# Kernel optimization log

Hardware: AMD Instinct MI355X
Metric: run time of the kernel (lower is better)

Reference implementation:

```python
import jax, jax.numpy as jnp
import numpy as np
import math

B, N, T, H, HEADS, FIN, NL_TR = 4, 256, 16, 128, 4, 2, 5
M = B * N
NEG = -1e9

def _sinusoidal(t, h):
    pos = jnp.arange(t, dtype=jnp.float32)[:, None]
    div = jnp.exp(jnp.arange(0, h, 2, dtype=jnp.float32) * (-math.log(10000.0) / h))
    pe = jnp.zeros((t, h), dtype=jnp.float32)
    pe = pe.at[:, 0::2].set(jnp.sin(pos * div))
    pe = pe.at[:, 1::2].set(jnp.cos(pos * div))
    return pe

def _gat(x, W, a_src, a_dst, b, E, m):
    # x: [T,M,F]; W: [F,heads,H]; E: [T,M,M] bool, E[t,i,j]=edge j->i; m: [T,M] bool
    h = jnp.einsum('tmf,fhd->tmhd', x, W)
    ss = jnp.einsum('tmhd,hd->tmh', h, a_src)  # source score per node
    sd = jnp.einsum('tmhd,hd->tmh', h, a_dst)  # dest score per node
    logits = jax.nn.leaky_relu(sd[:, :, None, :] + ss[:, None, :, :], 0.2)  # [T,i,j,h]
    logits = jnp.where(E[..., None], logits, NEG)
    alpha = jax.nn.softmax(logits, axis=2)  # segment-softmax over incoming edges
    out = jnp.einsum('tijh,tjhd->tihd', alpha, h).mean(axis=2) + b  # concat=False -> head mean + bias
    return jax.nn.relu(out) * m[..., None]

def _ln(x, s, b):
    mu = x.mean(-1, keepdims=True)
    v = ((x - mu) ** 2).mean(-1, keepdims=True)
    return (x - mu) / jnp.sqrt(v + 1e-5) * s + b

def _forward(ego_mask, positions, adjacency, gat1_W, gat1_asrc, gat1_adst, gat1_b, gatW, gat_asrc, gat_adst, gat_b, Wqkv, bqkv, Wo, bo, ln1_s, ln1_b, ln2_s, ln2_b, Wff1, bff1, Wff2, bff2):
    m = jnp.transpose(ego_mask, (1, 0, 2)).reshape(T, M)  # [T, B*N]
    eye = jnp.eye(M, dtype=bool)
    # edge j->i valid iff A[t,j,i]!=0 and both nodes masked; PyG GATConv adds self-loops
    E = ((jnp.swapaxes(adjacency, 1, 2) != 0) & m[:, :, None] & m[:, None, :]) | (eye[None] & m[:, :, None])
    x = _gat(positions, gat1_W, gat1_asrc, gat1_adst, gat1_b, E, m)
    for i in range(5):
        x = _gat(x, gatW[i], gat_asrc[i], gat_adst[i], gat_b[i], E, m)
    x_seq = jnp.transpose(x, (1, 0, 2)) + _sinusoidal(T, H)[None]  # [M, T, H]
    dh = H // HEADS
    scale = 1.0 / math.sqrt(dh)
    for l in range(NL_TR):
        q = (x_seq @ Wqkv[l, 0] + bqkv[l, 0]).reshape(M, T, HEADS, dh)
        k = (x_seq @ Wqkv[l, 1] + bqkv[l, 1]).reshape(M, T, HEADS, dh)
        v = (x_seq @ Wqkv[l, 2] + bqkv[l, 2]).reshape(M, T, HEADS, dh)
        sc = jnp.einsum('bqhd,bkhd->bhqk', q, k) * scale
        a = jax.nn.softmax(sc, axis=-1)
        o = jnp.einsum('bhqk,bkhd->bqhd', a, v).reshape(M, T, H) @ Wo[l] + bo[l]
        x_seq = _ln(x_seq + o, ln1_s[l], ln1_b[l])
        f = jax.nn.relu(x_seq @ Wff1[l] + bff1[l]) @ Wff2[l] + bff2[l]
        x_seq = _ln(x_seq + f, ln2_s[l], ln2_b[l])
    return x_seq.reshape(B, N, T, H)

def setup_inputs() -> dict:
    key = jax.random.key(0)
    ks = jax.random.split(key, 32)
    s = 0.05
    f32 = jnp.float32
    inp = {
        'ego_mask': jax.random.uniform(ks[0], (B, T, N)) < 0.95,
        'positions': jax.random.normal(ks[1], (T, M, FIN), dtype=f32),
        'adjacency': (jax.random.uniform(ks[2], (T, M, M)) < 0.02).astype(f32),
        'gat1_W': jax.random.normal(ks[3], (FIN, HEADS, H), dtype=f32) * s,
        'gat1_asrc': jax.random.normal(ks[4], (HEADS, H), dtype=f32) * s,
        'gat1_adst': jax.random.normal(ks[5], (HEADS, H), dtype=f32) * s,
        'gat1_b': jnp.zeros((H,), dtype=f32),
        'gatW': jax.random.normal(ks[6], (5, H, HEADS, H), dtype=f32) * s,
        'gat_asrc': jax.random.normal(ks[7], (5, HEADS, H), dtype=f32) * s,
        'gat_adst': jax.random.normal(ks[8], (5, HEADS, H), dtype=f32) * s,
        'gat_b': jnp.zeros((5, H), dtype=f32),
        'Wqkv': jax.random.normal(ks[9], (NL_TR, 3, H, H), dtype=f32) * s,
        'bqkv': jnp.zeros((NL_TR, 3, H), dtype=f32),
        'Wo': jax.random.normal(ks[10], (NL_TR, H, H), dtype=f32) * s,
        'bo': jnp.zeros((NL_TR, H), dtype=f32),
        'ln1_s': jnp.ones((NL_TR, H), dtype=f32),
        'ln1_b': jnp.zeros((NL_TR, H), dtype=f32),
        'ln2_s': jnp.ones((NL_TR, H), dtype=f32),
        'ln2_b': jnp.zeros((NL_TR, H), dtype=f32),
        'Wff1': jax.random.normal(ks[11], (NL_TR, H, 4 * H), dtype=f32) * s,
        'bff1': jnp.zeros((NL_TR, 4 * H), dtype=f32),
        'Wff2': jax.random.normal(ks[12], (NL_TR, 4 * H, H), dtype=f32) * s,
        'bff2': jnp.zeros((NL_TR, H), dtype=f32),
    }
    return inp

def reference(ego_mask, positions, adjacency, gat1_W, gat1_asrc, gat1_adst, gat1_b, gatW, gat_asrc, gat_adst, gat_b, Wqkv, bqkv, Wo, bo, ln1_s, ln1_b, ln2_s, ln2_b, Wff1, bff1, Wff2, bff2):
    return _forward(ego_mask, positions, adjacency, gat1_W, gat1_asrc, gat1_adst, gat1_b, gatW, gat_asrc, gat_adst, gat_b, Wqkv, bqkv, Wo, bo, ln1_s, ln1_b, ln2_s, ln2_b, Wff1, bff1, Wff2, bff2)
```

## Files before the change

### kernel.cpp

```cpp
#include <hip/hip_runtime.h>
#include <hip/hip_bf16.h>

#define TT 16
#define MM 1024
#define HDIM 128
#define NHEADS 4
#define NROWS (TT*MM)
#define MAXDEG 64

typedef __bf16 bf16x8 __attribute__((ext_vector_type(8)));
typedef float f32x4 __attribute__((ext_vector_type(4)));

__device__ __forceinline__ unsigned short f2b(float x) {
    unsigned u = __float_as_uint(x);
    u += 0x7fff + ((u >> 16) & 1);
    return (unsigned short)(u >> 16);
}
__device__ __forceinline__ float bu2f(unsigned short u) {
    return __uint_as_float(((unsigned)u) << 16);
}

__global__ __launch_bounds__(256) void k_init(const int* __restrict__ ego,
                                              float* __restrict__ mfl,
                                              int* __restrict__ cnt) {
    int idx = blockIdx.x * 256 + threadIdx.x;
    int t = idx >> 10, i = idx & 1023;
    int b = i >> 8, n = i & 255;
    mfl[idx] = ego[b * (TT * 256) + t * 256 + n] ? 1.f : 0.f;
    cnt[idx] = 0;
}

__global__ __launch_bounds__(256) void k_edges(const float* __restrict__ adj,
                                               const float* __restrict__ mfl,
                                               int* __restrict__ cnt,
                                               int* __restrict__ nbr) {
    int bid = blockIdx.x;
    int t = bid >> 6, jc = bid & 63;
    int tid = threadIdx.x;
    int i0 = tid * 4;
    int rowb = t * MM;
    float mi[4];
#pragma unroll
    for (int r = 0; r < 4; ++r) mi[r] = mfl[rowb + i0 + r];
    __shared__ float ms[16];
    if (tid < 16) ms[tid] = mfl[rowb + jc * 16 + tid];
    __syncthreads();
    const float* at = adj + (size_t)t * MM * MM;
#pragma unroll 4
    for (int jj = 0; jj < 16; ++jj) {
        int j = jc * 16 + jj;
        float4 a = *(const float4*)(at + (size_t)j * MM + i0);
        float mj = ms[jj];
#pragma unroll
        for (int r = 0; r < 4; ++r) {
            int i = i0 + r;
            bool e;
            if (j == i) e = (mi[r] != 0.f);
            else e = ((&a.x)[r] != 0.f) && (mj != 0.f) && (mi[r] != 0.f);
            if (e) {
                int row = rowb + i;
                int pos = atomicAdd(&cnt[row], 1);
                if (pos < MAXDEG) nbr[(size_t)row * MAXDEG + pos] = j;
            }
        }
    }
}

__global__ __launch_bounds__(256) void k_prep(const float* __restrict__ Wqkv,
                                              const float* __restrict__ Wo,
                                              const float* __restrict__ Wff1,
                                              const float* __restrict__ Wff2,
                                              const float* __restrict__ gW,
                                              unsigned short* __restrict__ Wb) {
    int o = blockIdx.x * 256 + threadIdx.x;
    const float* src; int cs;
    if (o < 122880) {
        int l = o / 24576, r = o % 24576;
        if (r < 6144) {
            int nt = r >> 8, rem = r & 255, ks = rem >> 6, lane = rem & 63;
            int mt = nt >> 3, cc = nt & 7;
            int k = ks * 32 + ((lane >> 4) << 3), c = cc * 16 + (lane & 15);
            src = Wqkv + ((size_t)(l * 3 + mt) * 128 + k) * 128 + c; cs = 128;
        } else if (r < 8192) {
            int u = r - 6144, nt = u >> 8, rem = u & 255, ks = rem >> 6, lane = rem & 63;
            int k = ks * 32 + ((lane >> 4) << 3), c = nt * 16 + (lane & 15);
            src = Wo + (size_t)l * 16384 + (size_t)k * 128 + c; cs = 128;
        } else if (r < 16384) {
            int u = r - 8192, nt = u >> 8, rem = u & 255, ks = rem >> 6, lane = rem & 63;
            int k = ks * 32 + ((lane >> 4) << 3), c = nt * 16 + (lane & 15);
            src = Wff1 + (size_t)l * 65536 + (size_t)k * 512 + c; cs = 512;
        } else {
            int u = r - 16384, nt = u >> 10, rem = u & 1023, ks = rem >> 6, lane = rem & 63;
            int k = ks * 32 + ((lane >> 4) << 3), c = nt * 16 + (lane & 15);
            src = Wff2 + (size_t)l * 65536 + (size_t)k * 128 + c; cs = 128;
        }
    } else {
        int u = o - 122880;
        int l = u >> 13, rr = u & 8191;
        int nt = rr >> 8, rem = rr & 255, ks = rem >> 6, lane = rem & 63;
        int k = ks * 32 + ((lane >> 4) << 3), c = nt * 16 + (lane & 15);
        src = gW + (size_t)l * 65536 + (size_t)k * 512 + c; cs = 512;
    }
    unsigned v[4];
#pragma unroll
    for (int j = 0; j < 4; ++j)
        v[j] = (unsigned)f2b(src[(2 * j) * (size_t)cs]) |
               ((unsigned)f2b(src[(2 * j + 1) * (size_t)cs]) << 16);
    *(uint4*)(Wb + (size_t)o * 8) = make_uint4(v[0], v[1], v[2], v[3]);
}

__global__ __launch_bounds__(128) void k_gat1(const float* __restrict__ x,
                                              const float* __restrict__ W,
                                              const float* __restrict__ asrc,
                                              const float* __restrict__ adst,
                                              unsigned short* __restrict__ h16,
                                              float* __restrict__ ss,
                                              float* __restrict__ sd) {
    int bid = blockIdx.x;
    int row = ((bid & 7) << 11) + (bid >> 3);
    int tid = threadIdx.x;
    float x0 = x[row * 2], x1 = x[row * 2 + 1];
    float s4[4], d4[4];
#pragma unroll
    for (int hh = 0; hh < 4; ++hh) {
        int o = hh * 128 + tid;
        float v = x0 * W[o] + x1 * W[512 + o];
        h16[(size_t)row * 512 + o] = f2b(v);
        s4[hh] = v * asrc[o];
        d4[hh] = v * adst[o];
    }
#pragma unroll
    for (int hh = 0; hh < 4; ++hh)
        for (int off = 32; off; off >>= 1) {
            s4[hh] += __shfl_down(s4[hh], off, 64);
            d4[hh] += __shfl_down(d4[hh], off, 64);
        }
    __shared__ float red[2][2][4];
    if ((tid & 63) == 0) {
        int w = tid >> 6;
#pragma unroll
        for (int hh = 0; hh < 4; ++hh) { red[w][0][hh] = s4[hh]; red[w][1][hh] = d4[hh]; }
    }
    __syncthreads();
    if (tid < 4) ss[row * 4 + tid] = red[0][0][tid] + red[1][0][tid];
    else if (tid < 8) sd[row * 4 + tid - 4] = red[0][1][tid - 4] + red[1][1][tid - 4];
}

__global__ __launch_bounds__(256, 2) void k_gat_h(const unsigned short* __restrict__ x16,
                                                  const unsigned short* __restrict__ Wg,
                                                  const float* __restrict__ asrc,
                                                  const float* __restrict__ adst,
                                                  unsigned short* __restrict__ h16,
                                                  float* __restrict__ ss,
                                                  float* __restrict__ sd) {
    __shared__ __align__(16) unsigned short xb[32 * 136];
    int bid = blockIdx.x;
    int row0 = (((bid & 7) << 6) + (bid >> 3)) * 32;
    int tid = threadIdx.x;
#pragma unroll
    for (int q = 0; q < 2; ++q) {
        int u = tid + q * 256;
        int rr = u >> 4, cc = (u & 15) * 8;
        *(uint4*)(xb + rr * 136 + cc) = *(const uint4*)(x16 + (size_t)(row0 + rr) * 128 + cc);
    }
    __syncthreads();
    const int lane = tid & 63, w = tid >> 6;
    const int mrow = lane & 15, quad = lane >> 4;
    float ps[2][4] = {{0,0,0,0},{0,0,0,0}}, pd[2][4] = {{0,0,0,0},{0,0,0,0}};
#pragma unroll
    for (int ib = 0; ib < 4; ++ib) {
        bf16x8 wb[8];
#pragma unroll
        for (int u = 0; u < 2; ++u) {
            int nt = w * 8 + ib * 2 + u;
#pragma unroll
            for (int ks = 0; ks < 4; ++ks)
                wb[u * 4 + ks] = *(const bf16x8*)(Wg + (size_t)((nt * 4 + ks) * 64 + lane) * 8);
        }
#pragma unroll
        for (int rg = 0; rg < 2; ++rg) {
            bf16x8 af[4];
#pragma unroll
            for (int ks = 0; ks < 4; ++ks)
                af[ks] = *(const bf16x8*)(xb + (rg * 16 + mrow) * 136 + ks * 32 + quad * 8);
            f32x4 acc[2];
            acc[0] = (f32x4){0.f, 0.f, 0.f, 0.f};
            acc[1] = (f32x4){0.f, 0.f, 0.f, 0.f};
#pragma unroll
            for (int u = 0; u < 2; ++u)
#pragma unroll
                for (int ks = 0; ks < 4; ++ks)
                    acc[u] = __builtin_amdgcn_mfma_f32_16x16x32_bf16(af[ks], wb[u * 4 + ks], acc[u], 0, 0, 0);
#pragma unroll
            for (int u = 0; u < 2; ++u) {
                int nt = w * 8 + ib * 2 + u, col = nt * 16 + mrow;
                float as_ = asrc[col], ad_ = adst[col];
#pragma unroll
                for (int r = 0; r < 4; ++r) {
                    float v = acc[u][r];
                    h16[(size_t)(row0 + rg * 16 + quad * 4 + r) * 512 + col] = f2b(v);
                    ps[rg][r] += v * as_; pd[rg][r] += v * ad_;
                }
            }
        }
    }
#pragma unroll
    for (int off = 1; off < 16; off <<= 1)
#pragma unroll
        for (int rg = 0; rg < 2; ++rg)
#pragma unroll
            for (int r = 0; r < 4; ++r) {
                ps[rg][r] += __shfl_xor(ps[rg][r], off, 64);
                pd[rg][r] += __shfl_xor(pd[rg][r], off, 64);
            }
    if (mrow == 0) {
#pragma unroll
        for (int rg = 0; rg < 2; ++rg)
#pragma unroll
            for (int r = 0; r < 4; ++r) {
                int row = row0 + rg * 16 + quad * 4 + r;
                ss[row * 4 + w] = ps[rg][r];
                sd[row * 4 + w] = pd[rg][r];
            }
    }
}

__global__ __launch_bounds__(256, 2) void k_agg(const unsigned short* __restrict__ h16,
                                                const float* __restrict__ ss,
                                                const float* __restrict__ sd,
                                                const int* __restrict__ cnt,
                                                const int* __restrict__ nbr,
                                                const float* __restrict__ mfl,
                                                const float* __restrict__ bias,
                                                unsigned short* __restrict__ xo16) {
    __shared__ float alB[4][MAXDEG][4];
    __shared__ int   nbB[4][MAXDEG];
    __shared__ __align__(16) float partB[4][512];
    int bid = blockIdx.x;
    int row0 = (((bid & 7) << 9) + (bid >> 3)) * 4;
    int tid = threadIdx.x;
    const int w = tid >> 6, lane = tid & 63;
    int row = row0 + w, t = row >> 10;
    bool valid = mfl[row] != 0.f;
    int c = 0;
    if (valid) { c = cnt[row]; if (c > MAXDEG) c = MAXDEG; }
    bool act = lane < c;
    int jreg = 0;
    float lg[4];
    if (act) {
        jreg = nbr[(size_t)row * MAXDEG + lane];
        int jr = t * MM + jreg;
#pragma unroll
        for (int hh = 0; hh < 4; ++hh) {
            float v = sd[row * 4 + hh] + ss[jr * 4 + hh];
            lg[hh] = v > 0.f ? v : 0.2f * v;
        }
    } else {
#pragma unroll
        for (int hh = 0; hh < 4; ++hh) lg[hh] = -1e30f;
    }
    float mx[4];
#pragma unroll
    for (int hh = 0; hh < 4; ++hh) mx[hh] = lg[hh];
#pragma unroll
    for (int off = 32; off; off >>= 1)
#pragma unroll
        for (int hh = 0; hh < 4; ++hh) mx[hh] = fmaxf(mx[hh], __shfl_xor(mx[hh], off, 64));
    float ev[4];
#pragma unroll
    for (int hh = 0; hh < 4; ++hh) ev[hh] = act ? __expf(lg[hh] - mx[hh]) : 0.f;
    float sm[4];
#pragma unroll
    for (int hh = 0; hh < 4; ++hh) sm[hh] = ev[hh];
#pragma unroll
    for (int off = 32; off; off >>= 1)
#pragma unroll
        for (int hh = 0; hh < 4; ++hh) sm[hh] += __shfl_xor(sm[hh], off, 64);
    if (act) {
        float4 a4 = make_float4(ev[0] / sm[0], ev[1] / sm[1], ev[2] / sm[2], ev[3] / sm[3]);
        *(float4*)&alB[w][lane][0] = a4;
        nbB[w][lane] = jreg;
    }
    __syncthreads();
    const int head = lane >> 4;
    float acc[8] = {0, 0, 0, 0, 0, 0, 0, 0};
    const unsigned short* hb = h16 + (size_t)t * MM * 512 + lane * 8;
    for (int n = 0; n < c; ++n) {
        int j = nbB[w][n];
        float a = alB[w][n][head];
        uint4 v = *(const uint4*)(hb + (size_t)j * 512);
        acc[0] += a * bu2f((unsigned short)(v.x & 0xffff));
        acc[1] += a * bu2f((unsigned short)(v.x >> 16));
        acc[2] += a * bu2f((unsigned short)(v.y & 0xffff));
        acc[3] += a * bu2f((unsigned short)(v.y >> 16));
        acc[4] += a * bu2f((unsigned short)(v.z & 0xffff));
        acc[5] += a * bu2f((unsigned short)(v.z >> 16));
        acc[6] += a * bu2f((unsigned short)(v.w & 0xffff));
        acc[7] += a * bu2f((unsigned short)(v.w >> 16));
    }
    *(float4*)&partB[w][lane * 8]     = make_float4(acc[0], acc[1], acc[2], acc[3]);
    *(float4*)&partB[w][lane * 8 + 4] = make_float4(acc[4], acc[5], acc[6], acc[7]);
    __syncthreads();
    {
        int d0 = lane * 2;
        unsigned outp = 0;
#pragma unroll
        for (int q = 0; q < 2; ++q) {
            int d = d0 + q;
            float v = 0.f;
            if (valid) {
                v = 0.25f * (partB[w][d] + partB[w][128 + d] + partB[w][256 + d] + partB[w][384 + d])
                    + bias[d];
                v = fmaxf(v, 0.f);
            }
            outp |= ((unsigned)f2b(v)) << (16 * q);
        }
        *(unsigned*)(xo16 + (size_t)row * 128 + d0) = outp;
    }
}

__device__ __forceinline__ void ln2x(float* xs, unsigned short* xbB,
                                     const float* s, const float* b) {
    int tid = threadIdx.x, lane = tid & 15;
#pragma unroll
    for (int half = 0; half < 2; ++half) {
        int rr = (tid >> 4) + half * 16;
        float* xr = xs + rr * 128;
        float sum = 0.f;
#pragma unroll
        for (int k2 = 0; k2 < 8; ++k2) sum += xr[lane + 16 * k2];
#pragma unroll
        for (int off = 8; off; off >>= 1) sum += __shfl_xor(sum, off, 16);
        float mean = sum * (1.f / 128.f);
        float vs = 0.f;
#pragma unroll
        for (int k2 = 0; k2 < 8; ++k2) { float d = xr[lane + 16 * k2] - mean; vs += d * d; }
#pragma unroll
        for (int off = 8; off; off >>= 1) vs += __shfl_xor(vs, off, 16);
        float rstd = rsqrtf(vs * (1.f / 128.f) + 1e-5f);
        unsigned short* xb = xbB + (rr >> 4) * 2176 + (rr & 15) * 136;
#pragma unroll
        for (int k2 = 0; k2 < 8; ++k2) {
            int d = lane + 16 * k2;
            float v = (xr[d] - mean) * rstd * s[d] + b[d];
            xr[d] = v;
            xb[d] = f2b(v);
        }
    }
    __syncthreads();
}

__global__ __launch_bounds__(256, 2) void k_tf(const unsigned short* __restrict__ xg,
        const unsigned short* __restrict__ Wb,
        const float* __restrict__ bqkv, const float* __restrict__ bo,
        const float* __restrict__ ln1s, const float* __restrict__ ln1b,
        const float* __restrict__ ln2s, const float* __restrict__ ln2b,
        const float* __restrict__ bff1, const float* __restrict__ bff2,
        float* __restrict__ out) {
    __shared__ __align__(16) float smem[16640];
    float* xs  = smem;
    float* sbB = smem + 4096;
    unsigned short* xbB  = (unsigned short*)(smem + 6144);
    unsigned short* qkvB = (unsigned short*)(smem + 8320);
    const int m0 = blockIdx.x * 2, tid = threadIdx.x;
    const int lane = tid & 63, w = tid >> 6;
    const int mrow = lane & 15, quad = lane >> 4;

    for (int idx = tid; idx < 4096; idx += 256) {
        int sq = idx >> 11, t = (idx >> 7) & 15, d = idx & 127, jj = d >> 1;
        float arg = (float)t * expf(-(float)(2 * jj) * (9.210340371976184f / 128.f));
        float pe = (d & 1) ? cosf(arg) : sinf(arg);
        xs[idx] = bu2f(xg[(size_t)t * (MM * HDIM) + (size_t)(m0 + sq) * HDIM + d]) + pe;
    }
    __syncthreads();
#pragma unroll
    for (int half = 0; half < 2; ++half) {
        int u = tid + half * 256;
        int rr = u >> 4, cc = (u & 15) * 8;
        const float* xp = xs + rr * 128 + cc;
        unsigned v[4];
#pragma unroll
        for (int j = 0; j < 4; ++j)
            v[j] = (unsigned)f2b(xp[2 * j]) | ((unsigned)f2b(xp[2 * j + 1]) << 16);
        *(uint4*)(xbB + (rr >> 4) * 2176 + (rr & 15) * 136 + cc) = make_uint4(v[0], v[1], v[2], v[3]);
    }
    __syncthreads();

    for (int l = 0; l < 5; ++l) {
        const unsigned short* Wl = Wb + (size_t)l * 196608;
        {
            bf16x8 af[2][4];
#pragma unroll
            for (int sid = 0; sid < 2; ++sid)
#pragma unroll
                for (int ks = 0; ks < 4; ++ks)
                    af[sid][ks] = *(const bf16x8*)(xbB + sid * 2176 + mrow * 136 + ks * 32 + quad * 8);
#pragma unroll
            for (int ib = 0; ib < 3; ++ib) {
                bf16x8 wb[8];
#pragma unroll
                for (int u = 0; u < 2; ++u) {
                    int nt = w * 6 + ib * 2 + u;
                    const unsigned short* bp = Wl + (size_t)(nt * 4) * 512 + lane * 8;
#pragma unroll
                    for (int ks = 0; ks < 4; ++ks)
                        wb[u * 4 + ks] = *(const bf16x8*)(bp + ks * 512);
                }
                f32x4 acc[2][2];
#pragma unroll
                for (int sid = 0; sid < 2; ++sid)
#pragma unroll
                    for (int u = 0; u < 2; ++u) acc[sid][u] = (f32x4){0.f, 0.f, 0.f, 0.f};
#pragma unroll
                for (int sid = 0; sid < 2; ++sid)
#pragma unroll
                    for (int u = 0; u < 2; ++u)
#pragma unroll
                        for (int ks = 0; ks < 4; ++ks)
                            acc[sid][u] = __builtin_amdgcn_mfma_f32_16x16x32_bf16(af[sid][ks], wb[u * 4 + ks], acc[sid][u], 0, 0, 0);
#pragma unroll
                for (int sid = 0; sid < 2; ++sid)
#pragma unroll
                    for (int u = 0; u < 2; ++u) {
                        int nt = w * 6 + ib * 2 + u, mt = nt >> 3, cc = nt & 7;
                        int col = cc * 16 + mrow;
                        float bb = bqkv[l * 384 + mt * 128 + col];
                        unsigned short* dst = qkvB + sid * 6528 + mt * 2176;
#pragma unroll
                        for (int r = 0; r < 4; ++r)
                            dst[(quad * 4 + r) * 136 + col] = f2b(acc[sid][u][r] + bb);
                    }
            }
        }
        __syncthreads();
        {
            int hh = tid >> 6, tq = (tid >> 2) & 15, tk0 = (tid & 3) * 4;
#pragma unroll
            for (int sid = 0; sid < 2; ++sid) {
                const unsigned short* qp = qkvB + sid * 6528 + tq * 136 + hh * 32;
                const unsigned short* kb = qkvB + sid * 6528 + 2176;
                float a[4] = {0.f, 0.f, 0.f, 0.f};
#pragma unroll
                for (int d4 = 0; d4 < 4; ++d4) {
                    uint4 qv = *(const uint4*)(qp + d4 * 8);
                    float qf[8];
                    qf[0] = bu2f((unsigned short)(qv.x & 0xffff)); qf[1] = bu2f((unsigned short)(qv.x >> 16));
                    qf[2] = bu2f((unsigned short)(qv.y & 0xffff)); qf[3] = bu2f((unsigned short)(qv.y >> 16));
                    qf[4] = bu2f((unsigned short)(qv.z & 0xffff)); qf[5] = bu2f((unsigned short)(qv.z >> 16));
                    qf[6] = bu2f((unsigned short)(qv.w & 0xffff)); qf[7] = bu2f((unsigned short)(qv.w >> 16));
#pragma unroll
                    for (int j = 0; j < 4; ++j) {
                        uint4 kv = *(const uint4*)(kb + (tk0 + j) * 136 + hh * 32 + d4 * 8);
                        a[j] += qf[0] * bu2f((unsigned short)(kv.x & 0xffff));
                        a[j] += qf[1] * bu2f((unsigned short)(kv.x >> 16));
                        a[j] += qf[2] * bu2f((unsigned short)(kv.y & 0xffff));
                        a[j] += qf[3] * bu2f((unsigned short)(kv.y >> 16));
                        a[j] += qf[4] * bu2f((unsigned short)(kv.z & 0xffff));
                        a[j] += qf[5] * bu2f((unsigned short)(kv.z >> 16));
                        a[j] += qf[6] * bu2f((unsigned short)(kv.w & 0xffff));
                        a[j] += qf[7] * bu2f((unsigned short)(kv.w >> 16));
                    }
                }
#pragma unroll
                for (int j = 0; j < 4; ++j)
                    sbB[sid * 1024 + (tk0 + j) * 64 + hh * 16 + tq] = a[j] * 0.17677669529663687f;
            }
        }
        __syncthreads();
        if (tid < 128) {
            float* sbp = sbB + (tid >> 6) * 1024;
            int cc = tid & 63;
            float mx = -1e30f;
#pragma unroll
            for (int u = 0; u < 16; ++u) mx = fmaxf(mx, sbp[u * 64 + cc]);
            float s = 0.f;
#pragma unroll
            for (int u = 0; u < 16; ++u) { float e = __expf(sbp[u * 64 + cc] - mx); sbp[u * 64 + cc] = e; s += e; }
            float inv = 1.f / s;
#pragma unroll
            for (int u = 0; u < 16; ++u) sbp[u * 64 + cc] *= inv;
        }
        __syncthreads();
        {
            int o = tid & 127, r0p = (tid >> 7) * 8, hh = o >> 5;
#pragma unroll
            for (int sid = 0; sid < 2; ++sid) {
                const unsigned short* vb = qkvB + sid * 6528 + 4352;
                const float* sb = sbB + sid * 1024;
                float accp[8] = {0, 0, 0, 0, 0, 0, 0, 0};
                for (int u = 0; u < 16; ++u) {
                    float vv = bu2f(vb[u * 136 + o]);
                    const float* pp = sb + u * 64 + hh * 16 + r0p;
#pragma unroll
                    for (int r = 0; r < 8; ++r) accp[r] += pp[r] * vv;
                }
#pragma unroll
                for (int r = 0; r < 8; ++r)
                    xbB[sid * 2176 + (r0p + r) * 136 + o] = f2b(accp[r]);
            }
        }
        __syncthreads();
        {
            bf16x8 af[2][4];
#pragma unroll
            for (int sid = 0; sid < 2; ++sid)
#pragma unroll
                for (int ks = 0; ks < 4; ++ks)
                    af[sid][ks] = *(const bf16x8*)(xbB + sid * 2176 + mrow * 136 + ks * 32 + quad * 8);
            const unsigned short* Ws = Wl + 49152;
            bf16x8 wb[8];
#pragma unroll
            for (int u = 0; u < 2; ++u) {
                int nt = w * 2 + u;
#pragma unroll
                for (int ks = 0; ks < 4; ++ks)
                    wb[u * 4 + ks] = *(const bf16x8*)(Ws + (size_t)((nt * 4 + ks) * 64 + lane) * 8);
            }
            f32x4 acc[2][2];
#pragma unroll
            for (int sid = 0; sid < 2; ++sid)
#pragma unroll
                for (int u = 0; u < 2; ++u) acc[sid][u] = (f32x4){0.f, 0.f, 0.f, 0.f};
#pragma unroll
            for (int sid = 0; sid < 2; ++sid)
#pragma unroll
                for (int u = 0; u < 2; ++u)
#pragma unroll
                    for (int ks = 0; ks < 4; ++ks)
                        acc[sid][u] = __builtin_amdgcn_mfma_f32_16x16x32_bf16(af[sid][ks], wb[u * 4 + ks], acc[sid][u], 0, 0, 0);
#pragma unroll
            for (int sid = 0; sid < 2; ++sid)
#pragma unroll
                for (int u = 0; u < 2; ++u) {
                    int col = (w * 2 + u) * 16 + mrow;
                    float bb = bo[l * 128 + col];
#pragma unroll
                    for (int r = 0; r < 4; ++r)
                        xs[sid * 2048 + (quad * 4 + r) * 128 + col] += acc[sid][u][r] + bb;
                }
        }
        __syncthreads();
        ln2x(xs, xbB, ln1s + l * 128, ln1b + l * 128);
        {
            bf16x8 af[2][4];
#pragma unroll
            for (int sid = 0; sid < 2; ++sid)
#pragma unroll
                for (int ks = 0; ks < 4; ++ks)
                    af[sid][ks] = *(const bf16x8*)(xbB + sid * 2176 + mrow * 136 + ks * 32 + quad * 8);
            const unsigned short* Ws = Wl + 65536;
#pragma unroll
            for (int ib = 0; ib < 4; ++ib) {
                bf16x8 wb[8];
#pragma unroll
                for (int u = 0; u < 2; ++u) {
                    int nt = w * 8 + ib * 2 + u;
#pragma unroll
                    for (int ks = 0; ks < 4; ++ks)
                        wb[u * 4 + ks] = *(const bf16x8*)(Ws + (size_t)((nt * 4 + ks) * 64 + lane) * 8);
                }
                f32x4 acc[2][2];
#pragma unroll
                for (int sid = 0; sid < 2; ++sid)
#pragma unroll
                    for (int u = 0; u < 2; ++u) acc[sid][u] = (f32x4){0.f, 0.f, 0.f, 0.f};
#pragma unroll
                for (int sid = 0; sid < 2; ++sid)
#pragma unroll
                    for (int u = 0; u < 2; ++u)
#pragma unroll
                        for (int ks = 0; ks < 4; ++ks)
                            acc[sid][u] = __builtin_amdgcn_mfma_f32_16x16x32_bf16(af[sid][ks], wb[u * 4 + ks], acc[sid][u], 0, 0, 0);
#pragma unroll
                for (int sid = 0; sid < 2; ++sid)
#pragma unroll
                    for (int u = 0; u < 2; ++u) {
                        int col = (w * 8 + ib * 2 + u) * 16 + mrow;
                        float bb = bff1[l * 512 + col];
                        unsigned short* hid16 = qkvB + sid * 8320;
#pragma unroll
                        for (int r = 0; r < 4; ++r) {
                            float v = fmaxf(acc[sid][u][r] + bb, 0.f);
                            hid16[(quad * 4 + r) * 520 + col] = f2b(v);
                        }
                    }
            }
        }
        __syncthreads();
        {
            f32x4 a[2][2];
#pragma unroll
            for (int sid = 0; sid < 2; ++sid)
#pragma unroll
                for (int u = 0; u < 2; ++u) a[sid][u] = (f32x4){0.f, 0.f, 0.f, 0.f};
            const unsigned short* Ws = Wl + 131072;
            int nt0 = w * 2, nt1 = w * 2 + 1;
#pragma unroll
            for (int kb = 0; kb < 4; ++kb) {
                bf16x8 w0[4], w1[4];
#pragma unroll
                for (int kk = 0; kk < 4; ++kk) {
                    int ks = kb * 4 + kk;
                    w0[kk] = *(const bf16x8*)(Ws + (size_t)((nt0 * 16 + ks) * 64 + lane) * 8);
                    w1[kk] = *(const bf16x8*)(Ws + (size_t)((nt1 * 16 + ks) * 64 + lane) * 8);
                }
#pragma unroll
                for (int sid = 0; sid < 2; ++sid) {
                    const unsigned short* hid16 = qkvB + sid * 8320;
#pragma unroll
                    for (int kk = 0; kk < 4; ++kk) {
                        int ks = kb * 4 + kk;
                        bf16x8 afb = *(const bf16x8*)(hid16 + mrow * 520 + ks * 32 + quad * 8);
                        a[sid][0] = __builtin_amdgcn_mfma_f32_16x16x32_bf16(afb, w0[kk], a[sid][0], 0, 0, 0);
                        a[sid][1] = __builtin_amdgcn_mfma_f32_16x16x32_bf16(afb, w1[kk], a[sid][1], 0, 0, 0);
                    }
                }
            }
            int col0 = nt0 * 16 + mrow, col1 = nt1 * 16 + mrow;
            float bb0 = bff2[l * 128 + col0], bb1 = bff2[l * 128 + col1];
#pragma unroll
            for (int sid = 0; sid < 2; ++sid)
#pragma unroll
                for (int r = 0; r < 4; ++r) {
                    xs[sid * 2048 + (quad * 4 + r) * 128 + col0] += a[sid][0][r] + bb0;
                    xs[sid * 2048 + (quad * 4 + r) * 128 + col1] += a[sid][1][r] + bb1;
                }
        }
        __syncthreads();
        ln2x(xs, xbB, ln2s + l * 128, ln2b + l * 128);
    }
    for (int idx = tid; idx < 4096; idx += 256)
        out[(size_t)m0 * 2048 + idx] = xs[idx];
}

extern "C" void kernel_launch(void* const* d_in, const int* in_sizes, int n_in,
                              void* d_out, int out_size, void* d_ws, size_t ws_size,
                              hipStream_t stream) {
    (void)in_sizes; (void)n_in; (void)out_size; (void)ws_size;
    const int*   ego  = (const int*)d_in[0];
    const float* pos  = (const float*)d_in[1];
    const float* adj  = (const float*)d_in[2];
    const float* g1W  = (const float*)d_in[3];
    const float* g1as = (const float*)d_in[4];
    const float* g1ad = (const float*)d_in[5];
    const float* g1b  = (const float*)d_in[6];
    const float* gW   = (const float*)d_in[7];
    const float* gas  = (const float*)d_in[8];
    const float* gad  = (const float*)d_in[9];
    const float* gb   = (const float*)d_in[10];
    const float* Wqkv = (const float*)d_in[11];
    const float* bqkv = (const float*)d_in[12];
    const float* Wo   = (const float*)d_in[13];
    const float* bo   = (const float*)d_in[14];
    const float* l1s  = (const float*)d_in[15];
    const float* l1b  = (const float*)d_in[16];
    const float* l2s  = (const float*)d_in[17];
    const float* l2b  = (const float*)d_in[18];
    const float* Wff1 = (const float*)d_in[19];
    const float* bff1 = (const float*)d_in[20];
    const float* Wff2 = (const float*)d_in[21];
    const float* bff2 = (const float*)d_in[22];

    unsigned short* x0  = (unsigned short*)d_ws;
    unsigned short* x1  = x0 + 2097152;
    unsigned short* h16 = x1 + 2097152;
    float* ssb = (float*)(h16 + 8388608);
    float* sdb = ssb + 65536;
    float* mfl = sdb + 65536;
    int*   cnt = (int*)(mfl + 16384);
    int*   nbr = cnt + 16384;
    unsigned short* Wb16 = (unsigned short*)(nbr + 1048576);
    unsigned short* Wg16 = Wb16 + 983040;

    k_prep<<<640, 256, 0, stream>>>(Wqkv, Wo, Wff1, Wff2, gW, Wb16);
    k_init<<<64, 256, 0, stream>>>(ego, mfl, cnt);
    k_edges<<<1024, 256, 0, stream>>>(adj, mfl, cnt, nbr);

    k_gat1<<<NROWS, 128, 0, stream>>>(pos, g1W, g1as, g1ad, h16, ssb, sdb);
    k_agg<<<4096, 256, 0, stream>>>(h16, ssb, sdb, cnt, nbr, mfl, g1b, x0);

    unsigned short* xin = x0; unsigned short* xout = x1;
    for (int L = 0; L < 5; ++L) {
        k_gat_h<<<512, 256, 0, stream>>>(xin, Wg16 + (size_t)L * 65536,
                                         gas + L * 512, gad + L * 512, h16, ssb, sdb);
        k_agg<<<4096, 256, 0, stream>>>(h16, ssb, sdb, cnt, nbr, mfl, gb + L * 128, xout);
        unsigned short* tmp = xin; xin = xout; xout = tmp;
    }

    k_tf<<<512, 256, 0, stream>>>(xin, Wb16, bqkv, bo, l1s, l1b, l2s, l2b,
                                  bff1, bff2, (float*)d_out);
}
```

Measured before the change: 491.9 us.

## Software-pipeline weight fragment loads across GEMM stages in transformer kernel

Weight fragments for each GEMM are now prefetched into registers ahead of use. Loads for the next block are issued before the current MFMA block, before preceding syncs, and across layers. This hides global/L2 latency of the weight reads behind compute and barriers. The cost is many more live VGPRs (four 8-vector buffers), which under launch_bounds(256,2) could cause spills.

```diff
diff --git a/kernel.cpp b/kernel.cpp
--- a/kernel.cpp
+++ b/kernel.cpp
@@ -350,6 +350,37 @@
     __syncthreads();
 }
 
+#define LDB(dst, base, n0, n1) do { \
+    const unsigned short* p0_ = (base) + ((size_t)(n0) * 2048 + lane * 8); \
+    const unsigned short* p1_ = (base) + ((size_t)(n1) * 2048 + lane * 8); \
+    dst[0] = *(const bf16x8*)(p0_);        dst[1] = *(const bf16x8*)(p0_ + 512); \
+    dst[2] = *(const bf16x8*)(p0_ + 1024); dst[3] = *(const bf16x8*)(p0_ + 1536); \
+    dst[4] = *(const bf16x8*)(p1_);        dst[5] = *(const bf16x8*)(p1_ + 512); \
+    dst[6] = *(const bf16x8*)(p1_ + 1024); dst[7] = *(const bf16x8*)(p1_ + 1536); \
+} while (0)
+
+#define LDB2(dst, base, n0, n1, kb) do { \
+    const unsigned short* p0_ = (base) + ((size_t)((n0) * 16 + (kb) * 4) * 512 + lane * 8); \
+    const unsigned short* p1_ = (base) + ((size_t)((n1) * 16 + (kb) * 4) * 512 + lane * 8); \
+    dst[0] = *(const bf16x8*)(p0_);        dst[1] = *(const bf16x8*)(p0_ + 512); \
+    dst[2] = *(const bf16x8*)(p0_ + 1024); dst[3] = *(const bf16x8*)(p0_ + 1536); \
+    dst[4] = *(const bf16x8*)(p1_);        dst[5] = *(const bf16x8*)(p1_ + 512); \
+    dst[6] = *(const bf16x8*)(p1_ + 1024); dst[7] = *(const bf16x8*)(p1_ + 1536); \
+} while (0)
+
+#define MF2(wv) do { \
+    _Pragma("unroll") for (int s_ = 0; s_ < 2; ++s_) \
+    _Pragma("unroll") for (int u_ = 0; u_ < 2; ++u_) \
+    _Pragma("unroll") for (int k_ = 0; k_ < 4; ++k_) \
+        acc[s_][u_] = __builtin_amdgcn_mfma_f32_16x16x32_bf16(af[s_][k_], wv[u_ * 4 + k_], acc[s_][u_], 0, 0, 0); \
+} while (0)
+
+#define ZACC do { \
+    _Pragma("unroll") for (int s_ = 0; s_ < 2; ++s_) \
+    _Pragma("unroll") for (int u_ = 0; u_ < 2; ++u_) \
+        acc[s_][u_] = (f32x4){0.f, 0.f, 0.f, 0.f}; \
+} while (0)
+
 __global__ __launch_bounds__(256, 2) void k_tf(const unsigned short* __restrict__ xg,
         const unsigned short* __restrict__ Wb,
         const float* __restrict__ bqkv, const float* __restrict__ bo,
@@ -366,6 +397,10 @@
     const int lane = tid & 63, w = tid >> 6;
     const int mrow = lane & 15, quad = lane >> 4;
 
+    bf16x8 wq[8], nxt[8], pw[8], pwo[8];
+
+    LDB(wq, Wb, w * 6, w * 6 + 1);
+
     for (int idx = tid; idx < 4096; idx += 256) {
         int sq = idx >> 11, t = (idx >> 7) & 15, d = idx & 127, jj = d >> 1;
         float arg = (float)t * expf(-(float)(2 * jj) * (9.210340371976184f / 128.f));
@@ -395,29 +430,15 @@
 #pragma unroll
                 for (int ks = 0; ks < 4; ++ks)
                     af[sid][ks] = *(const bf16x8*)(xbB + sid * 2176 + mrow * 136 + ks * 32 + quad * 8);
+            LDB(nxt, Wl, w * 6 + 2, w * 6 + 3);
+            LDB(pwo, Wl + 49152, w * 2, w * 2 + 1);
+            f32x4 acc[2][2];
 #pragma unroll
             for (int ib = 0; ib < 3; ++ib) {
-                bf16x8 wb[8];
-#pragma unroll
-                for (int u = 0; u < 2; ++u) {
-                    int nt = w * 6 + ib * 2 + u;
-                    const unsigned short* bp = Wl + (size_t)(nt * 4) * 512 + lane * 8;
-#pragma unroll
-                    for (int ks = 0; ks < 4; ++ks)
-                        wb[u * 4 + ks] = *(const bf16x8*)(bp + ks * 512);
-                }
-                f32x4 acc[2][2];
-#pragma unroll
-                for (int sid = 0; sid < 2; ++sid)
-#pragma unroll
-                    for (int u = 0; u < 2; ++u) acc[sid][u] = (f32x4){0.f, 0.f, 0.f, 0.f};
-#pragma unroll
-                for (int sid = 0; sid < 2; ++sid)
-#pragma unroll
-                    for (int u = 0; u < 2; ++u)
-#pragma unroll
-                        for (int ks = 0; ks < 4; ++ks)
-                            acc[sid][u] = __builtin_amdgcn_mfma_f32_16x16x32_bf16(af[sid][ks], wb[u * 4 + ks], acc[sid][u], 0, 0, 0);
+                ZACC;
+                if (ib == 0)      { MF2(wq); LDB(wq, Wl, w * 6 + 4, w * 6 + 5); }
+                else if (ib == 1) { MF2(nxt); }
+                else              { MF2(wq); }
 #pragma unroll
                 for (int sid = 0; sid < 2; ++sid)
 #pragma unroll
@@ -507,27 +528,10 @@
 #pragma unroll
                 for (int ks = 0; ks < 4; ++ks)
                     af[sid][ks] = *(const bf16x8*)(xbB + sid * 2176 + mrow * 136 + ks * 32 + quad * 8);
-            const unsigned short* Ws = Wl + 49152;
-            bf16x8 wb[8];
-#pragma unroll
-            for (int u = 0; u < 2; ++u) {
-                int nt = w * 2 + u;
-#pragma unroll
-                for (int ks = 0; ks < 4; ++ks)
-                    wb[u * 4 + ks] = *(const bf16x8*)(Ws + (size_t)((nt * 4 + ks) * 64 + lane) * 8);
-            }
+            LDB(pw, Wl + 65536, w * 8, w * 8 + 1);
             f32x4 acc[2][2];
-#pragma unroll
-            for (int sid = 0; sid < 2; ++sid)
-#pragma unroll
-                for (int u = 0; u < 2; ++u) acc[sid][u] = (f32x4){0.f, 0.f, 0.f, 0.f};
-#pragma unroll
-            for (int sid = 0; sid < 2; ++sid)
-#pragma unroll
-                for (int u = 0; u < 2; ++u)
-#pragma unroll
-                    for (int ks = 0; ks < 4; ++ks)
-                        acc[sid][u] = __builtin_amdgcn_mfma_f32_16x16x32_bf16(af[sid][ks], wb[u * 4 + ks], acc[sid][u], 0, 0, 0);
+            ZACC;
+            MF2(pwo);
 #pragma unroll
             for (int sid = 0; sid < 2; ++sid)
 #pragma unroll
@@ -549,28 +553,16 @@
                 for (int ks = 0; ks < 4; ++ks)
                     af[sid][ks] = *(const bf16x8*)(xbB + sid * 2176 + mrow * 136 + ks * 32 + quad * 8);
             const unsigned short* Ws = Wl + 65536;
+            LDB(nxt, Ws, w * 8 + 2, w * 8 + 3);
+            LDB2(pwo, Wl + 131072, w * 2, w * 2 + 1, 0);
+            f32x4 acc[2][2];
 #pragma unroll
             for (int ib = 0; ib < 4; ++ib) {
-                bf16x8 wb[8];
-#pragma unroll
-                for (int u = 0; u < 2; ++u) {
-                    int nt = w * 8 + ib * 2 + u;
-#pragma unroll
-                    for (int ks = 0; ks < 4; ++ks)
-                        wb[u * 4 + ks] = *(const bf16x8*)(Ws + (size_t)((nt * 4 + ks) * 64 + lane) * 8);
-                }
-                f32x4 acc[2][2];
-#pragma unroll
-                for (int sid = 0; sid < 2; ++sid)
-#pragma unroll
-                    for (int u = 0; u < 2; ++u) acc[sid][u] = (f32x4){0.f, 0.f, 0.f, 0.f};
-#pragma unroll
-                for (int sid = 0; sid < 2; ++sid)
-#pragma unroll
-                    for (int u = 0; u < 2; ++u)
-#pragma unroll
-                        for (int ks = 0; ks < 4; ++ks)
-                            acc[sid][u] = __builtin_amdgcn_mfma_f32_16x16x32_bf16(af[sid][ks], wb[u * 4 + ks], acc[sid][u], 0, 0, 0);
+                ZACC;
+                if (ib == 0)      { MF2(pw);  LDB(pw,  Ws, w * 8 + 4, w * 8 + 5); }
+                else if (ib == 1) { MF2(nxt); LDB(nxt, Ws, w * 8 + 6, w * 8 + 7); }
+                else if (ib == 2) { MF2(pw); }
+                else              { MF2(nxt); }
 #pragma unroll
                 for (int sid = 0; sid < 2; ++sid)
 #pragma unroll
@@ -595,15 +587,10 @@
                 for (int u = 0; u < 2; ++u) a[sid][u] = (f32x4){0.f, 0.f, 0.f, 0.f};
             const unsigned short* Ws = Wl + 131072;
             int nt0 = w * 2, nt1 = w * 2 + 1;
+            LDB2(pw, Ws, nt0, nt1, 1);
+            if (l < 4) LDB(wq, Wl + 196608, w * 6, w * 6 + 1);
 #pragma unroll
             for (int kb = 0; kb < 4; ++kb) {
-                bf16x8 w0[4], w1[4];
-#pragma unroll
-                for (int kk = 0; kk < 4; ++kk) {
-                    int ks = kb * 4 + kk;
-                    w0[kk] = *(const bf16x8*)(Ws + (size_t)((nt0 * 16 + ks) * 64 + lane) * 8);
-                    w1[kk] = *(const bf16x8*)(Ws + (size_t)((nt1 * 16 + ks) * 64 + lane) * 8);
-                }
 #pragma unroll
                 for (int sid = 0; sid < 2; ++sid) {
                     const unsigned short* hid16 = qkvB + sid * 8320;
@@ -611,10 +598,17 @@
                     for (int kk = 0; kk < 4; ++kk) {
                         int ks = kb * 4 + kk;
                         bf16x8 afb = *(const bf16x8*)(hid16 + mrow * 520 + ks * 32 + quad * 8);
-                        a[sid][0] = __builtin_amdgcn_mfma_f32_16x16x32_bf16(afb, w0[kk], a[sid][0], 0, 0, 0);
-                        a[sid][1] = __builtin_amdgcn_mfma_f32_16x16x32_bf16(afb, w1[kk], a[sid][1], 0, 0, 0);
+                        if (kb == 0 || kb == 2) {
+                            a[sid][0] = __builtin_amdgcn_mfma_f32_16x16x32_bf16(afb, pwo[kk],     a[sid][0], 0, 0, 0);
+                            a[sid][1] = __builtin_amdgcn_mfma_f32_16x16x32_bf16(afb, pwo[4 + kk], a[sid][1], 0, 0, 0);
+                        } else {
+                            a[sid][0] = __builtin_amdgcn_mfma_f32_16x16x32_bf16(afb, pw[kk],      a[sid][0], 0, 0, 0);
+                            a[sid][1] = __builtin_amdgcn_mfma_f32_16x16x32_bf16(afb, pw[4 + kk],  a[sid][1], 0, 0, 0);
+                        }
                     }
                 }
+                if (kb == 0)      { LDB2(pwo, Ws, nt0, nt1, 2); }
+                else if (kb == 1) { LDB2(pw,  Ws, nt0, nt1, 3); }
             }
             int col0 = nt0 * 16 + mrow, col1 = nt1 * 16 + mrow;
             float bb0 = bff2[l * 128 + col0], bb1 = bff2[l * 128 + col1];
```

Measured after the change: 496.0 us. Within noise of the previous version (+0.8%).
